# Performance work log

Hardware: AMD Instinct MI355X
Metric: run time of the kernel (lower is better)

## Reference

```python
import jax, jax.numpy as jnp
import numpy as np
from jax.ops import segment_sum

N = 100000
E = 1600000


def gcn_conv(x, W, b, src, dst, n_nodes):
    # PyG GCNConv: linear transform, then symmetric-normalized scatter-add.
    # src/dst already include self-loops; edge weights are all ones.
    h = x @ W  # [N, out]
    deg = segment_sum(jnp.ones(src.shape[0], dtype=x.dtype), dst, num_segments=n_nodes)
    dinv = jnp.where(deg > 0, jax.lax.rsqrt(jnp.maximum(deg, 1e-12)), 0.0).astype(x.dtype)
    norm = dinv[src] * dinv[dst]  # [E]
    msg = h[src] * norm[:, None]  # gather + scale, [E, out]
    out = segment_sum(msg, dst, num_segments=n_nodes)  # scatter-add
    return out + b


def setup_inputs() -> dict:
    key = jax.random.key(0)
    k1, k2, k3, k4 = jax.random.split(key, 4)
    x = jax.random.normal(k1, (N, 128), dtype=jnp.float32)
    edge_index = jax.random.randint(k2, (2, E), 0, N, dtype=jnp.int32)
    # Glorot-ish scaled weights
    W1 = jax.random.normal(k3, (128, 64), dtype=jnp.float32) * (1.0 / np.sqrt(128))
    b1 = jnp.zeros((64,), dtype=jnp.float32)
    W2 = jax.random.normal(k4, (64, 32), dtype=jnp.float32) * (1.0 / np.sqrt(64))
    b2 = jnp.zeros((32,), dtype=jnp.float32)
    return {"x": x, "edge_index": edge_index, "W1": W1, "b1": b1, "W2": W2, "b2": b2}


def reference(x, edge_index, W1, b1, W2, b2):
    n = x.shape[0]
    # add self-loops (PyG default add_self_loops=True)
    loops = jnp.arange(n, dtype=edge_index.dtype)
    src = jnp.concatenate([edge_index[0], loops])
    dst = jnp.concatenate([edge_index[1], loops])
    h = gcn_conv(x, W1, b1, src, dst, n)
    h = jax.nn.relu(h)
    out = gcn_conv(h, W2, b2, src, dst, n)
    return out
```

## Files before the change

kernel.cpp:

```cpp
#include <hip/hip_runtime.h>
#include <hip/hip_fp16.h>

#define BS 256
#define BSHIFT 9
#define BNODES (1 << BSHIFT)
#define NBKT 256
#define CAP 12288
#define CHUNK 4096

typedef _Float16 f16x8 __attribute__((ext_vector_type(8)));
typedef float f32x4 __attribute__((ext_vector_type(4)));


__global__ __launch_bounds__(BS) void k_prep(const int* __restrict__ src,
                                             const int* __restrict__ dst,
                                             int* __restrict__ gcursor,
                                             int* __restrict__ binned, int E,
                                             const float* __restrict__ X,
                                             const float* __restrict__ W,
                                             __half* __restrict__ H, int n,
                                             int nchunks) {
    __shared__ int sh[NBKT];
    __shared__ int sbase[NBKT];
    __shared__ __align__(16) _Float16 sB[64 * 128];
    int t = threadIdx.x;
    if (blockIdx.x < nchunks) {
        sh[t] = 0;
        __syncthreads();
        int cbase = blockIdx.x * CHUNK;
        int sv[CHUNK / BS], dv[CHUNK / BS], rv[CHUNK / BS];
#pragma unroll
        for (int j = 0; j < CHUNK / BS; ++j) {
            int e = cbase + j * BS + t;
            rv[j] = -1;
            if (e < E) {
                sv[j] = src[e];
                dv[j] = dst[e];
                rv[j] = atomicAdd(&sh[dv[j] >> BSHIFT], 1);
            }
        }
        __syncthreads();
        sbase[t] = sh[t] ? atomicAdd(&gcursor[t], sh[t]) : 0;
        __syncthreads();
#pragma unroll
        for (int j = 0; j < CHUNK / BS; ++j) {
            if (rv[j] >= 0) {
                int b = dv[j] >> BSHIFT;
                binned[(size_t)b * CAP + sbase[b] + rv[j]] =
                    sv[j] | ((dv[j] & (BNODES - 1)) << 17);
            }
        }
        return;
    }
    constexpr int K = 128, COLS = 64;
    constexpr int KC = K / 8;
    constexpr int SWZ = 15;
    constexpr int NT = COLS / 16;
    int bid = blockIdx.x - nchunks;
    for (int idx = t; idx < COLS * KC; idx += BS) {
        int c = idx / KC, k8 = idx % KC;
        f16x8 v;
#pragma unroll
        for (int j = 0; j < 8; ++j) v[j] = (_Float16)W[(k8 * 8 + j) * COLS + c];
        *(f16x8*)&sB[c * K + ((k8 ^ (c & SWZ)) * 8)] = v;
    }
    __syncthreads();
    int w = t >> 6, lane = t & 63;
    int lm = lane & 15, q = lane >> 4;
    int row_m0 = bid * 128 + w * 32;
    f32x4 acc[2][NT];
#pragma unroll
    for (int tm = 0; tm < 2; ++tm)
#pragma unroll
        for (int tn = 0; tn < NT; ++tn) acc[tm][tn] = (f32x4){0.f, 0.f, 0.f, 0.f};
#pragma unroll
    for (int kk = 0; kk < K / 32; ++kk) {
        int k0 = kk * 32 + q * 8;
        f16x8 af[2], bf[NT];
#pragma unroll
        for (int tm = 0; tm < 2; ++tm) {
            int row = row_m0 + tm * 16 + lm;
            int rl = row < n ? row : (n - 1);
            const float4* xp = (const float4*)X + ((size_t)rl * K + k0) / 4;
            float4 a = xp[0], b = xp[1];
            f16x8 v;
            v[0] = (_Float16)a.x; v[1] = (_Float16)a.y;
            v[2] = (_Float16)a.z; v[3] = (_Float16)a.w;
            v[4] = (_Float16)b.x; v[5] = (_Float16)b.y;
            v[6] = (_Float16)b.z; v[7] = (_Float16)b.w;
            af[tm] = v;
        }
#pragma unroll
        for (int tn = 0; tn < NT; ++tn) {
            int c = tn * 16 + lm;
            bf[tn] = *(const f16x8*)&sB[c * K + (((kk * 4 + q) ^ (c & SWZ)) * 8)];
        }
#pragma unroll
        for (int tm = 0; tm < 2; ++tm)
#pragma unroll
            for (int tn = 0; tn < NT; ++tn)
                acc[tm][tn] = __builtin_amdgcn_mfma_f32_16x16x32_f16(af[tm], bf[tn],
                                                                     acc[tm][tn], 0, 0, 0);
    }
#pragma unroll
    for (int tm = 0; tm < 2; ++tm) {
#pragma unroll
        for (int r = 0; r < 4; ++r) {
            int row = row_m0 + tm * 16 + q * 4 + r;
            if (row < n) {
#pragma unroll
                for (int tn = 0; tn < NT; ++tn) {
                    int col = tn * 16 + lm;
                    H[(size_t)row * COLS + col] = __float2half_rn(acc[tm][tn][r]);
                }
            }
        }
    }
}


__global__ __launch_bounds__(BS) void k_build(const int* __restrict__ binned,
                                              const int* __restrict__ cnts,
                                              int2* __restrict__ rowptr2,
                                              float* __restrict__ dinv,
                                              int* __restrict__ csr, int n) {
    __shared__ int h[BNODES];
    __shared__ int rp[BNODES];
    __shared__ int cur[BNODES];
    __shared__ int ws[4];
    int t = threadIdx.x;
    int bkt = blockIdx.x;
    int node0 = bkt << BSHIFT;
    int nn = min(BNODES, n - node0);
#pragma unroll
    for (int i = t; i < BNODES; i += BS) h[i] = 0;
    __syncthreads();
    int cnt = cnts[bkt];
    const int* eb = binned + (size_t)bkt * CAP;
    for (int e = t; e < cnt; e += BS) atomicAdd(&h[eb[e] >> 17], 1);
    __syncthreads();
    int i0 = 2 * t;
    int v0 = h[i0], v1 = h[i0 + 1];
    int pair = v0 + v1;
    int lane = t & 63, w = t >> 6;
    int incl = pair;
#pragma unroll
    for (int off = 1; off < 64; off <<= 1) {
        int u = __shfl_up(incl, off);
        if (lane >= off) incl += u;
    }
    if (lane == 63) ws[w] = incl;
    __syncthreads();
    int woff = 0;
    for (int q = 0; q < w; ++q) woff += ws[q];
    int excl = woff + incl - pair;
    int cb = bkt * (CAP + BNODES);
    int r0 = cb + excl + i0;
    int r1 = r0 + v0 + 1;
    rp[i0] = r0; rp[i0 + 1] = r1;
    cur[i0] = 1; cur[i0 + 1] = 1;
    if (i0 < nn) {
        rowptr2[node0 + i0] = make_int2(r0, r1);
        dinv[node0 + i0] = rsqrtf((float)(v0 + 1));
        csr[r0] = node0 + i0;
    }
    if (i0 + 1 < nn) {
        rowptr2[node0 + i0 + 1] = make_int2(r1, r1 + v1 + 1);
        dinv[node0 + i0 + 1] = rsqrtf((float)(v1 + 1));
        csr[r1] = node0 + i0 + 1;
    }
    __syncthreads();
    for (int e = t; e < cnt; e += BS) {
        int p = eb[e];
        int li = p >> 17;
        int r = atomicAdd(&cur[li], 1);
        csr[rp[li] + r] = p & 0x1FFFF;
    }
}


__device__ __forceinline__ void acc_fma(float4 raw, __half2 d, __half2& p0, __half2& p1,
                                        __half2& p2, __half2& p3) {
    const __half2* u = (const __half2*)&raw;
    p0 = __hfma2(u[0], d, p0); p1 = __hfma2(u[1], d, p1);
    p2 = __hfma2(u[2], d, p2); p3 = __hfma2(u[3], d, p3);
}

__global__ __launch_bounds__(BS) void k_aggmm(const __half* __restrict__ hsrc,
                                              const int* __restrict__ csr,
                                              const int2* __restrict__ rowptr2,
                                              const float* __restrict__ dinv,
                                              const float* __restrict__ b1,
                                              const float* __restrict__ W2,
                                              __half* __restrict__ h2, int n) {
    __shared__ float sW2[64 * 32];
    __shared__ float sB1[64];
    __shared__ float sU[(BS / 64) * 2 * 64];
    int t = threadIdx.x;
    for (int i = t; i < 64 * 32; i += BS) sW2[i] = W2[i];
    if (t < 64) sB1[t] = b1[t];
    __syncthreads();

    int npairs = (n + 1) / 2;
    int wib = t >> 6;
    int wid = blockIdx.x * (BS / 64) + wib;
    if (wid >= npairs) return;
    int lane = t & 63;
    int half = lane >> 5, hl = lane & 31;
    int node = wid * 2 + half;
    bool valid = node < n;
    int b = 0, e = 0;
    if (valid) { int2 be = rowptr2[node]; b = be.x; e = be.y; }
    int slot = hl >> 3, fq = hl & 7;
    __half2 pA0 = __float2half2_rn(0.f), pA1 = pA0, pA2 = pA0, pA3 = pA0;
    __half2 pB0 = pA0, pB1 = pA0, pB2 = pA0, pB3 = pA0;
    for (int c = b; c < e; c += 32) {
        int m = e - c;
        if (m > 32) m = 32;
        int sv = (hl < m) ? csr[c + hl] : 0;
        float dsv = dinv[sv];
        int j = 0;
        for (; j + 7 < m; j += 8) {
            int s0 = __shfl(sv, j + slot, 32);
            float d0 = __shfl(dsv, j + slot, 32);
            int s1 = __shfl(sv, j + 4 + slot, 32);
            float d1 = __shfl(dsv, j + 4 + slot, 32);
            float4 r0 = *((const float4*)(hsrc + (size_t)s0 * 64) + fq);
            float4 r1 = *((const float4*)(hsrc + (size_t)s1 * 64) + fq);
            acc_fma(r0, __float2half2_rn(d0), pA0, pA1, pA2, pA3);
            acc_fma(r1, __float2half2_rn(d1), pB0, pB1, pB2, pB3);
        }
        for (; j < m; j += 4) {
            int js = j + slot;
            int s = __shfl(sv, js < m ? js : 0, 32);
            float d = __shfl(dsv, js < m ? js : 0, 32);
            if (js < m) {
                float4 r0 = *((const float4*)(hsrc + (size_t)s * 64) + fq);
                acc_fma(r0, __float2half2_rn(d), pA0, pA1, pA2, pA3);
            }
        }
    }
    float2 f0 = __half22float2(pA0), f1 = __half22float2(pA1);
    float2 f2 = __half22float2(pA2), f3 = __half22float2(pA3);
    float2 g0 = __half22float2(pB0), g1v = __half22float2(pB1);
    float2 g2 = __half22float2(pB2), g3 = __half22float2(pB3);
    float a0 = f0.x + g0.x, a1 = f0.y + g0.y, a2 = f1.x + g1v.x, a3 = f1.y + g1v.y;
    float a4 = f2.x + g2.x, a5 = f2.y + g2.y, a6 = f3.x + g3.x, a7 = f3.y + g3.y;
    a0 += __shfl_down(a0, 16); a1 += __shfl_down(a1, 16);
    a2 += __shfl_down(a2, 16); a3 += __shfl_down(a3, 16);
    a4 += __shfl_down(a4, 16); a5 += __shfl_down(a5, 16);
    a6 += __shfl_down(a6, 16); a7 += __shfl_down(a7, 16);
    a0 += __shfl_down(a0, 8);  a1 += __shfl_down(a1, 8);
    a2 += __shfl_down(a2, 8);  a3 += __shfl_down(a3, 8);
    a4 += __shfl_down(a4, 8);  a5 += __shfl_down(a5, 8);
    a6 += __shfl_down(a6, 8);  a7 += __shfl_down(a7, 8);

    if (valid && hl < 8) {
        float dv = dinv[node];
        float* up = &sU[(wib * 2 + half) * 64 + hl * 8];
        up[0] = fmaxf(a0 * dv + sB1[hl * 8 + 0], 0.f);
        up[1] = fmaxf(a1 * dv + sB1[hl * 8 + 1], 0.f);
        up[2] = fmaxf(a2 * dv + sB1[hl * 8 + 2], 0.f);
        up[3] = fmaxf(a3 * dv + sB1[hl * 8 + 3], 0.f);
        up[4] = fmaxf(a4 * dv + sB1[hl * 8 + 4], 0.f);
        up[5] = fmaxf(a5 * dv + sB1[hl * 8 + 5], 0.f);
        up[6] = fmaxf(a6 * dv + sB1[hl * 8 + 6], 0.f);
        up[7] = fmaxf(a7 * dv + sB1[hl * 8 + 7], 0.f);
    }
    int nodeSel = lane >> 5;
    int mvnode = wid * 2 + nodeSel;
    if (mvnode < n) {
        const float* u = &sU[(wib * 2 + nodeSel) * 64];
        int cc = lane & 31;
        float acc = 0.f;
#pragma unroll
        for (int k = 0; k < 64; ++k) acc = fmaf(u[k], sW2[k * 32 + cc], acc);
        h2[(size_t)mvnode * 32 + cc] = __float2half_rn(acc * dinv[mvnode]);
    }
}


__global__ __launch_bounds__(BS) void k_agg32(const __half* __restrict__ h,
                                              const int* __restrict__ csr,
                                              const int2* __restrict__ rowptr2,
                                              const float* __restrict__ dinv,
                                              const float* __restrict__ bias,
                                              float* __restrict__ out, int n) {
    int wid = (blockIdx.x * BS + threadIdx.x) >> 6;
    int lane = threadIdx.x & 63;
    int half = lane >> 5, hl = lane & 31;
    int node = wid * 2 + half;
    bool valid = node < n;
    int b = 0, e = 0;
    if (valid) { int2 be = rowptr2[node]; b = be.x; e = be.y; }
    int slot = hl >> 2, fq = hl & 3;
    float a0 = 0.f, a1 = 0.f, a2 = 0.f, a3 = 0.f;
    float a4 = 0.f, a5 = 0.f, a6 = 0.f, a7 = 0.f;
    for (int c = b; c < e; c += 32) {
        int m = e - c;
        if (m > 32) m = 32;
        int sv = (hl < m) ? csr[c + hl] : 0;
        int j = 0;
        for (; j + 15 < m; j += 16) {
            int s0 = __shfl(sv, j + slot, 32);
            int s1 = __shfl(sv, j + 8 + slot, 32);
            float4 r0 = *((const float4*)(h + (size_t)s0 * 32) + fq);
            float4 r1 = *((const float4*)(h + (size_t)s1 * 32) + fq);
            const __half2* u0 = (const __half2*)&r0;
            const __half2* u1 = (const __half2*)&r1;
            float2 q0 = __half22float2(u0[0]), q1 = __half22float2(u0[1]);
            float2 q2 = __half22float2(u0[2]), q3 = __half22float2(u0[3]);
            a0 += q0.x; a1 += q0.y; a2 += q1.x; a3 += q1.y;
            a4 += q2.x; a5 += q2.y; a6 += q3.x; a7 += q3.y;
            q0 = __half22float2(u1[0]); q1 = __half22float2(u1[1]);
            q2 = __half22float2(u1[2]); q3 = __half22float2(u1[3]);
            a0 += q0.x; a1 += q0.y; a2 += q1.x; a3 += q1.y;
            a4 += q2.x; a5 += q2.y; a6 += q3.x; a7 += q3.y;
        }
        for (; j < m; j += 8) {
            int js = j + slot;
            int s = __shfl(sv, js < m ? js : 0, 32);
            if (js < m) {
                float4 r0 = *((const float4*)(h + (size_t)s * 32) + fq);
                const __half2* u0 = (const __half2*)&r0;
                float2 q0 = __half22float2(u0[0]), q1 = __half22float2(u0[1]);
                float2 q2 = __half22float2(u0[2]), q3 = __half22float2(u0[3]);
                a0 += q0.x; a1 += q0.y; a2 += q1.x; a3 += q1.y;
                a4 += q2.x; a5 += q2.y; a6 += q3.x; a7 += q3.y;
            }
        }
    }
    a0 += __shfl_down(a0, 16); a1 += __shfl_down(a1, 16);
    a2 += __shfl_down(a2, 16); a3 += __shfl_down(a3, 16);
    a4 += __shfl_down(a4, 16); a5 += __shfl_down(a5, 16);
    a6 += __shfl_down(a6, 16); a7 += __shfl_down(a7, 16);
    a0 += __shfl_down(a0, 8);  a1 += __shfl_down(a1, 8);
    a2 += __shfl_down(a2, 8);  a3 += __shfl_down(a3, 8);
    a4 += __shfl_down(a4, 8);  a5 += __shfl_down(a5, 8);
    a6 += __shfl_down(a6, 8);  a7 += __shfl_down(a7, 8);
    a0 += __shfl_down(a0, 4);  a1 += __shfl_down(a1, 4);
    a2 += __shfl_down(a2, 4);  a3 += __shfl_down(a3, 4);
    a4 += __shfl_down(a4, 4);  a5 += __shfl_down(a5, 4);
    a6 += __shfl_down(a6, 4);  a7 += __shfl_down(a7, 4);
    if (valid && hl < 4) {
        float dv = dinv[node];
        const float4* bp = (const float4*)bias + hl * 2;
        float4 b0 = bp[0], b1v = bp[1];
        float4 o0 = make_float4(a0 * dv + b0.x, a1 * dv + b0.y,
                                a2 * dv + b0.z, a3 * dv + b0.w);
        float4 o1 = make_float4(a4 * dv + b1v.x, a5 * dv + b1v.y,
                                a6 * dv + b1v.z, a7 * dv + b1v.w);
        float4* op = (float4*)(out + (size_t)node * 32 + hl * 8);
        op[0] = o0; op[1] = o1;
    }
}


extern "C" void kernel_launch(void* const* d_in, const int* in_sizes, int n_in,
                              void* d_out, int out_size, void* d_ws, size_t ws_size,
                              hipStream_t stream) {
    const float* x  = (const float*)d_in[0];
    const int* eidx = (const int*)d_in[1];
    const float* W1 = (const float*)d_in[2];
    const float* b1 = (const float*)d_in[3];
    const float* W2 = (const float*)d_in[4];
    const float* b2 = (const float*)d_in[5];
    float* out = (float*)d_out;

    int n = in_sizes[0] / 128;
    int E = in_sizes[1] / 2;
    const int* srcA = eidx;
    const int* dstA = eidx + E;

    char* p = (char*)d_ws;
    auto alloc = [&](size_t bytes) {
        char* q = p;
        p += (bytes + 255) & ~(size_t)255;
        return q;
    };
    int2*   rowptr2 = (int2*)alloc((size_t)n * 8);
    float*  dinv    = (float*)alloc((size_t)n * 4);
    int*    gcursor = (int*)alloc(NBKT * 4);
    int*    binned  = (int*)alloc((size_t)NBKT * CAP * 4);
    int*    csr     = (int*)alloc((size_t)NBKT * (CAP + BNODES) * 4);
    __half* h1      = (__half*)alloc((size_t)n * 64 * 2);
    __half* h2      = (__half*)alloc((size_t)n * 32 * 2);

    int nchunks  = (E + CHUNK - 1) / CHUNK;
    int nbuckets = (n + BNODES - 1) / BNODES;
    int nblk     = (n + 127) / 128;
    int npairs   = (n + 1) / 2;
    int aggblk   = (npairs + (BS / 64) - 1) / (BS / 64);

    hipMemsetAsync(gcursor, 0, NBKT * 4, stream);
    k_prep<<<nchunks + nblk, BS, 0, stream>>>(srcA, dstA, gcursor, binned, E,
                                              x, W1, h1, n, nchunks);
    k_build<<<nbuckets, BS, 0, stream>>>(binned, gcursor, rowptr2, dinv, csr, n);
    k_aggmm<<<aggblk, BS, 0, stream>>>(h1, csr, rowptr2, dinv, b1, W2, h2, n);
    k_agg32<<<aggblk, BS, 0, stream>>>(h2, csr, rowptr2, dinv, b2, out, n);
}
```

Measured before the change: 223.9 us.

## Replace bucketed binning CSR build with global-atomic degree count, scan, and placement

Replaces the two-pass bucketed construction (block-local binning into fixed-capacity buckets, then per-bucket local histogram and placement in LDS) with a classic CSR build. Degrees are counted with global atomics, a two-kernel prefix scan builds rowptr, dinv and the self-loop entries, and edges are placed through per-node global atomic cursors. This drops the fixed bucket capacity and padded CSR layout and shrinks intermediate storage. In exchange it uses about 3.2M scattered global atomics instead of LDS atomics, adds a full memset and two extra launches, and makes the CSR order within a row nondeterministic.

```diff
diff --git a/kernel.cpp b/kernel.cpp
--- a/kernel.cpp
+++ b/kernel.cpp
@@ -2,53 +2,26 @@
 #include <hip/hip_fp16.h>
 
 #define BS 256
-#define BSHIFT 9
-#define BNODES (1 << BSHIFT)
-#define NBKT 256
-#define CAP 12288
-#define CHUNK 4096
+#define EPB (BS * 8)
 
 typedef _Float16 f16x8 __attribute__((ext_vector_type(8)));
 typedef float f32x4 __attribute__((ext_vector_type(4)));
 
 
-__global__ __launch_bounds__(BS) void k_prep(const int* __restrict__ src,
-                                             const int* __restrict__ dst,
-                                             int* __restrict__ gcursor,
-                                             int* __restrict__ binned, int E,
-                                             const float* __restrict__ X,
+__global__ __launch_bounds__(BS) void k_prep(const float* __restrict__ X,
                                              const float* __restrict__ W,
                                              __half* __restrict__ H, int n,
-                                             int nchunks) {
-    __shared__ int sh[NBKT];
-    __shared__ int sbase[NBKT];
+                                             int nblk,
+                                             const int* __restrict__ dst,
+                                             int* __restrict__ deg, int E) {
     __shared__ __align__(16) _Float16 sB[64 * 128];
     int t = threadIdx.x;
-    if (blockIdx.x < nchunks) {
-        sh[t] = 0;
-        __syncthreads();
-        int cbase = blockIdx.x * CHUNK;
-        int sv[CHUNK / BS], dv[CHUNK / BS], rv[CHUNK / BS];
-#pragma unroll
-        for (int j = 0; j < CHUNK / BS; ++j) {
-            int e = cbase + j * BS + t;
-            rv[j] = -1;
-            if (e < E) {
-                sv[j] = src[e];
-                dv[j] = dst[e];
-                rv[j] = atomicAdd(&sh[dv[j] >> BSHIFT], 1);
-            }
-        }
-        __syncthreads();
-        sbase[t] = sh[t] ? atomicAdd(&gcursor[t], sh[t]) : 0;
-        __syncthreads();
-#pragma unroll
-        for (int j = 0; j < CHUNK / BS; ++j) {
-            if (rv[j] >= 0) {
-                int b = dv[j] >> BSHIFT;
-                binned[(size_t)b * CAP + sbase[b] + rv[j]] =
-                    sv[j] | ((dv[j] & (BNODES - 1)) << 17);
-            }
+    if (blockIdx.x >= nblk) {
+        int base = (blockIdx.x - nblk) * EPB;
+#pragma unroll
+        for (int j = 0; j < 8; ++j) {
+            int e = base + j * BS + t;
+            if (e < E) atomicAdd(&deg[dst[e]], 1);
         }
         return;
     }
@@ -56,7 +29,7 @@
     constexpr int KC = K / 8;
     constexpr int SWZ = 15;
     constexpr int NT = COLS / 16;
-    int bid = blockIdx.x - nchunks;
+    int bid = blockIdx.x;
     for (int idx = t; idx < COLS * KC; idx += BS) {
         int c = idx / KC, k8 = idx % KC;
         f16x8 v;
@@ -119,31 +92,47 @@
 }
 
 
-__global__ __launch_bounds__(BS) void k_build(const int* __restrict__ binned,
-                                              const int* __restrict__ cnts,
+__global__ __launch_bounds__(BS) void k_scan1(const int* __restrict__ deg,
+                                              int* __restrict__ bsum, int n) {
+    __shared__ int red[BS / 64];
+    int b = blockIdx.x, t = threadIdx.x;
+    int base = b * 1024 + t * 4;
+    int s = 0;
+#pragma unroll
+    for (int i = 0; i < 4; ++i) {
+        int v = base + i;
+        if (v < n) s += deg[v] + 1;
+    }
+#pragma unroll
+    for (int off = 32; off; off >>= 1) s += __shfl_down(s, off);
+    if ((t & 63) == 0) red[t >> 6] = s;
+    __syncthreads();
+    if (t == 0) bsum[b] = red[0] + red[1] + red[2] + red[3];
+}
+
+
+__global__ __launch_bounds__(BS) void k_scan2(const int* __restrict__ deg,
+                                              const int* __restrict__ bsum, int nb2,
                                               int2* __restrict__ rowptr2,
                                               float* __restrict__ dinv,
-                                              int* __restrict__ csr, int n) {
-    __shared__ int h[BNODES];
-    __shared__ int rp[BNODES];
-    __shared__ int cur[BNODES];
-    __shared__ int ws[4];
-    int t = threadIdx.x;
-    int bkt = blockIdx.x;
-    int node0 = bkt << BSHIFT;
-    int nn = min(BNODES, n - node0);
-#pragma unroll
-    for (int i = t; i < BNODES; i += BS) h[i] = 0;
+                                              int* __restrict__ csr,
+                                              int* __restrict__ cur, int n) {
+    __shared__ int sb[256];
+    __shared__ int ws[BS / 64];
+    int b = blockIdx.x, t = threadIdx.x;
+    if (t < nb2) sb[t] = bsum[t];
     __syncthreads();
-    int cnt = cnts[bkt];
-    const int* eb = binned + (size_t)bkt * CAP;
-    for (int e = t; e < cnt; e += BS) atomicAdd(&h[eb[e] >> 17], 1);
-    __syncthreads();
-    int i0 = 2 * t;
-    int v0 = h[i0], v1 = h[i0 + 1];
-    int pair = v0 + v1;
+    int boff = 0;
+    for (int q = 0; q < b; ++q) boff += sb[q];
+    int base = b * 1024 + t * 4;
+    int v0 = 0, v1 = 0, v2 = 0, v3 = 0;
+    if (base + 0 < n) v0 = deg[base + 0] + 1;
+    if (base + 1 < n) v1 = deg[base + 1] + 1;
+    if (base + 2 < n) v2 = deg[base + 2] + 1;
+    if (base + 3 < n) v3 = deg[base + 3] + 1;
+    int tsum = v0 + v1 + v2 + v3;
     int lane = t & 63, w = t >> 6;
-    int incl = pair;
+    int incl = tsum;
 #pragma unroll
     for (int off = 1; off < 64; off <<= 1) {
         int u = __shfl_up(incl, off);
@@ -153,28 +142,50 @@
     __syncthreads();
     int woff = 0;
     for (int q = 0; q < w; ++q) woff += ws[q];
-    int excl = woff + incl - pair;
-    int cb = bkt * (CAP + BNODES);
-    int r0 = cb + excl + i0;
-    int r1 = r0 + v0 + 1;
-    rp[i0] = r0; rp[i0 + 1] = r1;
-    cur[i0] = 1; cur[i0 + 1] = 1;
-    if (i0 < nn) {
-        rowptr2[node0 + i0] = make_int2(r0, r1);
-        dinv[node0 + i0] = rsqrtf((float)(v0 + 1));
-        csr[r0] = node0 + i0;
-    }
-    if (i0 + 1 < nn) {
-        rowptr2[node0 + i0 + 1] = make_int2(r1, r1 + v1 + 1);
-        dinv[node0 + i0 + 1] = rsqrtf((float)(v1 + 1));
-        csr[r1] = node0 + i0 + 1;
-    }
-    __syncthreads();
-    for (int e = t; e < cnt; e += BS) {
-        int p = eb[e];
-        int li = p >> 17;
-        int r = atomicAdd(&cur[li], 1);
-        csr[rp[li] + r] = p & 0x1FFFF;
+    int st = boff + woff + incl - tsum;
+    if (base + 0 < n) {
+        rowptr2[base + 0] = make_int2(st, st + v0);
+        dinv[base + 0] = rsqrtf((float)v0);
+        csr[st] = base + 0;
+        cur[base + 0] = st + 1;
+    }
+    st += v0;
+    if (base + 1 < n) {
+        rowptr2[base + 1] = make_int2(st, st + v1);
+        dinv[base + 1] = rsqrtf((float)v1);
+        csr[st] = base + 1;
+        cur[base + 1] = st + 1;
+    }
+    st += v1;
+    if (base + 2 < n) {
+        rowptr2[base + 2] = make_int2(st, st + v2);
+        dinv[base + 2] = rsqrtf((float)v2);
+        csr[st] = base + 2;
+        cur[base + 2] = st + 1;
+    }
+    st += v2;
+    if (base + 3 < n) {
+        rowptr2[base + 3] = make_int2(st, st + v3);
+        dinv[base + 3] = rsqrtf((float)v3);
+        csr[st] = base + 3;
+        cur[base + 3] = st + 1;
+    }
+}
+
+
+__global__ __launch_bounds__(BS) void k_place(const int* __restrict__ src,
+                                              const int* __restrict__ dst,
+                                              int* __restrict__ cur,
+                                              int* __restrict__ csr, int E) {
+    int t = threadIdx.x;
+    int base = blockIdx.x * EPB;
+#pragma unroll
+    for (int j = 0; j < 8; ++j) {
+        int e = base + j * BS + t;
+        if (e < E) {
+            int pos = atomicAdd(&cur[dst[e]], 1);
+            csr[pos] = src[e];
+        }
     }
 }
 
@@ -380,22 +391,24 @@
     };
     int2*   rowptr2 = (int2*)alloc((size_t)n * 8);
     float*  dinv    = (float*)alloc((size_t)n * 4);
-    int*    gcursor = (int*)alloc(NBKT * 4);
-    int*    binned  = (int*)alloc((size_t)NBKT * CAP * 4);
-    int*    csr     = (int*)alloc((size_t)NBKT * (CAP + BNODES) * 4);
+    int*    deg     = (int*)alloc((size_t)n * 4);
+    int*    cur     = (int*)alloc((size_t)n * 4);
+    int*    bsum    = (int*)alloc(256 * 4);
+    int*    csr     = (int*)alloc(((size_t)E + n + 256) * 4);
     __half* h1      = (__half*)alloc((size_t)n * 64 * 2);
     __half* h2      = (__half*)alloc((size_t)n * 32 * 2);
 
-    int nchunks  = (E + CHUNK - 1) / CHUNK;
-    int nbuckets = (n + BNODES - 1) / BNODES;
-    int nblk     = (n + 127) / 128;
-    int npairs   = (n + 1) / 2;
-    int aggblk   = (npairs + (BS / 64) - 1) / (BS / 64);
-
-    hipMemsetAsync(gcursor, 0, NBKT * 4, stream);
-    k_prep<<<nchunks + nblk, BS, 0, stream>>>(srcA, dstA, gcursor, binned, E,
-                                              x, W1, h1, n, nchunks);
-    k_build<<<nbuckets, BS, 0, stream>>>(binned, gcursor, rowptr2, dinv, csr, n);
+    int nblk   = (n + 127) / 128;
+    int dblk   = (E + EPB - 1) / EPB;
+    int nb2    = (n + 1023) / 1024;
+    int npairs = (n + 1) / 2;
+    int aggblk = (npairs + (BS / 64) - 1) / (BS / 64);
+
+    hipMemsetAsync(deg, 0, (size_t)n * 4, stream);
+    k_prep<<<nblk + dblk, BS, 0, stream>>>(x, W1, h1, n, nblk, dstA, deg, E);
+    k_scan1<<<nb2, BS, 0, stream>>>(deg, bsum, n);
+    k_scan2<<<nb2, BS, 0, stream>>>(deg, bsum, nb2, rowptr2, dinv, csr, cur, n);
+    k_place<<<dblk, BS, 0, stream>>>(srcA, dstA, cur, csr, E);
     k_aggmm<<<aggblk, BS, 0, stream>>>(h1, csr, rowptr2, dinv, b1, W2, h2, n);
     k_agg32<<<aggblk, BS, 0, stream>>>(h2, csr, rowptr2, dinv, b2, out, n);
 }
```

Result: slower. 391.7 us (+74.9%).

## Split first-layer GEMM across binning and CSR-build kernels for better overlap

Applied to the files above, without the earlier changes.

Moves the X@W1 GEMM into a shared device helper and divides its row blocks between the edge-binning kernel and the CSR-build kernel. The build kernel has only about 196 bucket blocks, which leaves many CUs idle, so half the GEMM tiles now fill that gap while binning gets a lighter load. The trade-off is that the build kernel now reserves the 16KB GEMM shared-memory tile in every block, which may lower its occupancy.

```diff
diff --git a/kernel.cpp b/kernel.cpp
--- a/kernel.cpp
+++ b/kernel.cpp
@@ -12,51 +12,15 @@
 typedef float f32x4 __attribute__((ext_vector_type(4)));
 
 
-__global__ __launch_bounds__(BS) void k_prep(const int* __restrict__ src,
-                                             const int* __restrict__ dst,
-                                             int* __restrict__ gcursor,
-                                             int* __restrict__ binned, int E,
-                                             const float* __restrict__ X,
-                                             const float* __restrict__ W,
-                                             __half* __restrict__ H, int n,
-                                             int nchunks) {
-    __shared__ int sh[NBKT];
-    __shared__ int sbase[NBKT];
-    __shared__ __align__(16) _Float16 sB[64 * 128];
-    int t = threadIdx.x;
-    if (blockIdx.x < nchunks) {
-        sh[t] = 0;
-        __syncthreads();
-        int cbase = blockIdx.x * CHUNK;
-        int sv[CHUNK / BS], dv[CHUNK / BS], rv[CHUNK / BS];
-#pragma unroll
-        for (int j = 0; j < CHUNK / BS; ++j) {
-            int e = cbase + j * BS + t;
-            rv[j] = -1;
-            if (e < E) {
-                sv[j] = src[e];
-                dv[j] = dst[e];
-                rv[j] = atomicAdd(&sh[dv[j] >> BSHIFT], 1);
-            }
-        }
-        __syncthreads();
-        sbase[t] = sh[t] ? atomicAdd(&gcursor[t], sh[t]) : 0;
-        __syncthreads();
-#pragma unroll
-        for (int j = 0; j < CHUNK / BS; ++j) {
-            if (rv[j] >= 0) {
-                int b = dv[j] >> BSHIFT;
-                binned[(size_t)b * CAP + sbase[b] + rv[j]] =
-                    sv[j] | ((dv[j] & (BNODES - 1)) << 17);
-            }
-        }
-        return;
-    }
+__device__ __forceinline__ void mgemm_body(const float* __restrict__ X,
+                                           const float* __restrict__ W,
+                                           __half* __restrict__ H, int n, int bid,
+                                           _Float16* sB) {
     constexpr int K = 128, COLS = 64;
     constexpr int KC = K / 8;
     constexpr int SWZ = 15;
     constexpr int NT = COLS / 16;
-    int bid = blockIdx.x - nchunks;
+    int t = threadIdx.x;
     for (int idx = t; idx < COLS * KC; idx += BS) {
         int c = idx / KC, k8 = idx % KC;
         f16x8 v;
@@ -119,16 +83,69 @@
 }
 
 
-__global__ __launch_bounds__(BS) void k_build(const int* __restrict__ binned,
+__global__ __launch_bounds__(BS) void k_prepA(const int* __restrict__ src,
+                                              const int* __restrict__ dst,
+                                              int* __restrict__ gcursor,
+                                              int* __restrict__ binned, int E,
+                                              const float* __restrict__ X,
+                                              const float* __restrict__ W,
+                                              __half* __restrict__ H, int n,
+                                              int nchunks) {
+    __shared__ int sh[NBKT];
+    __shared__ int sbase[NBKT];
+    __shared__ __align__(16) _Float16 sB[64 * 128];
+    int t = threadIdx.x;
+    if (blockIdx.x < nchunks) {
+        sh[t] = 0;
+        __syncthreads();
+        int cbase = blockIdx.x * CHUNK;
+        int sv[CHUNK / BS], dv[CHUNK / BS], rv[CHUNK / BS];
+#pragma unroll
+        for (int j = 0; j < CHUNK / BS; ++j) {
+            int e = cbase + j * BS + t;
+            rv[j] = -1;
+            if (e < E) {
+                sv[j] = src[e];
+                dv[j] = dst[e];
+                rv[j] = atomicAdd(&sh[dv[j] >> BSHIFT], 1);
+            }
+        }
+        __syncthreads();
+        sbase[t] = sh[t] ? atomicAdd(&gcursor[t], sh[t]) : 0;
+        __syncthreads();
+#pragma unroll
+        for (int j = 0; j < CHUNK / BS; ++j) {
+            if (rv[j] >= 0) {
+                int b = dv[j] >> BSHIFT;
+                binned[(size_t)b * CAP + sbase[b] + rv[j]] =
+                    sv[j] | ((dv[j] & (BNODES - 1)) << 17);
+            }
+        }
+        return;
+    }
+    mgemm_body(X, W, H, n, blockIdx.x - nchunks, sB);
+}
+
+
+__global__ __launch_bounds__(BS) void k_prepB(const int* __restrict__ binned,
                                               const int* __restrict__ cnts,
                                               int2* __restrict__ rowptr2,
                                               float* __restrict__ dinv,
-                                              int* __restrict__ csr, int n) {
+                                              int* __restrict__ csr, int n,
+                                              int nbuckets,
+                                              const float* __restrict__ X,
+                                              const float* __restrict__ W,
+                                              __half* __restrict__ H, int mgA) {
     __shared__ int h[BNODES];
     __shared__ int rp[BNODES];
     __shared__ int cur[BNODES];
     __shared__ int ws[4];
+    __shared__ __align__(16) _Float16 sB[64 * 128];
     int t = threadIdx.x;
+    if (blockIdx.x >= nbuckets) {
+        mgemm_body(X, W, H, n, blockIdx.x - nbuckets + mgA, sB);
+        return;
+    }
     int bkt = blockIdx.x;
     int node0 = bkt << BSHIFT;
     int nn = min(BNODES, n - node0);
@@ -389,13 +406,16 @@
     int nchunks  = (E + CHUNK - 1) / CHUNK;
     int nbuckets = (n + BNODES - 1) / BNODES;
     int nblk     = (n + 127) / 128;
+    int mgA      = nblk / 2;
     int npairs   = (n + 1) / 2;
     int aggblk   = (npairs + (BS / 64) - 1) / (BS / 64);
 
     hipMemsetAsync(gcursor, 0, NBKT * 4, stream);
-    k_prep<<<nchunks + nblk, BS, 0, stream>>>(srcA, dstA, gcursor, binned, E,
+    k_prepA<<<nchunks + mgA, BS, 0, stream>>>(srcA, dstA, gcursor, binned, E,
                                               x, W1, h1, n, nchunks);
-    k_build<<<nbuckets, BS, 0, stream>>>(binned, gcursor, rowptr2, dinv, csr, n);
+    k_prepB<<<nbuckets + (nblk - mgA), BS, 0, stream>>>(binned, gcursor, rowptr2,
+                                                        dinv, csr, n, nbuckets,
+                                                        x, W1, h1, mgA);
     k_aggmm<<<aggblk, BS, 0, stream>>>(h1, csr, rowptr2, dinv, b1, W2, h2, n);
     k_agg32<<<aggblk, BS, 0, stream>>>(h2, csr, rowptr2, dinv, b2, out, n);
 }
```

New measurement: 220.6 us. About the same (-1.5%).
